# Kernel optimization log

Hardware: AMD Instinct MI355X
Metric: run time of the kernel (lower is better)

## Reference

```python
import jax, jax.numpy as jnp
import numpy as np

RES = 7          # POOLER_RESOLUTION
SR = 2           # POOLER_SAMPLING_RATIO
SCALES = (0.25, 0.125, 0.0625, 0.03125)
CANONICAL_SCALE = 224.0
CANONICAL_LEVEL = 4.0
K_MIN, K_MAX = 2.0, 5.0  # -log2(SCALES[0]), -log2(SCALES[-1])


def setup_inputs() -> dict:
    key = jax.random.key(0)
    ks = jax.random.split(key, 9)
    feat0 = jax.random.normal(ks[0], (2, 256, 200, 200), dtype=jnp.float32)
    feat1 = jax.random.normal(ks[1], (2, 256, 100, 100), dtype=jnp.float32)
    feat2 = jax.random.normal(ks[2], (2, 256, 50, 50), dtype=jnp.float32)
    feat3 = jax.random.normal(ks[3], (2, 256, 25, 25), dtype=jnp.float32)
    R = 512
    x1 = jax.random.uniform(ks[4], (R,)) * 600.0
    y1 = jax.random.uniform(ks[5], (R,)) * 600.0
    w = 16.0 + jax.random.uniform(ks[6], (R,)) * 500.0
    h = 16.0 + jax.random.uniform(ks[7], (R,)) * 500.0
    boxes = jnp.stack([x1, y1, x1 + w, y1 + h], axis=1).astype(jnp.float32)
    batch_idx = jax.random.randint(ks[8], (R,), 0, 2, dtype=jnp.int32)
    return {"feat0": feat0, "feat1": feat1, "feat2": feat2, "feat3": feat3,
            "boxes": boxes, "batch_idx": batch_idx}


def _map_levels(boxes):
    # LevelMapper: floor(k0 + log2(sqrt(area)/224 + eps)), clamp to [k_min,k_max], shift
    area = jnp.maximum(boxes[:, 2] - boxes[:, 0], 0.0) * jnp.maximum(boxes[:, 3] - boxes[:, 1], 0.0)
    s = jnp.sqrt(area)
    lvl = jnp.floor(CANONICAL_LEVEL + jnp.log2(s / CANONICAL_SCALE + 1e-6))
    return (jnp.clip(lvl, K_MIN, K_MAX) - K_MIN).astype(jnp.int32)


def _roi_align(feat, boxes, batch_idx, scale):
    # feat: [B,C,H,W]; boxes: [R,4] (x1,y1,x2,y2) in image coords; ROIAlign (aligned=False)
    H, W = feat.shape[2], feat.shape[3]
    x1 = boxes[:, 0] * scale
    y1 = boxes[:, 1] * scale
    x2 = boxes[:, 2] * scale
    y2 = boxes[:, 3] * scale
    roi_w = jnp.maximum(x2 - x1, 1.0)
    roi_h = jnp.maximum(y2 - y1, 1.0)
    bin_w = roi_w / RES
    bin_h = roi_h / RES
    # sample-point offsets within the roi, in bin units: [RES*SR]
    p = (jnp.arange(RES, dtype=jnp.float32)[:, None]
         + (jnp.arange(SR, dtype=jnp.float32)[None, :] + 0.5) / SR).reshape(-1)
    ys = y1[:, None] + p[None, :] * bin_h[:, None]   # [R,S]
    xs = x1[:, None] + p[None, :] * bin_w[:, None]   # [R,S]
    valid_y = (ys >= -1.0) & (ys <= float(H))
    valid_x = (xs >= -1.0) & (xs <= float(W))
    yc = jnp.clip(ys, 0.0, float(H - 1))
    xc = jnp.clip(xs, 0.0, float(W - 1))
    y0 = jnp.floor(yc).astype(jnp.int32)
    x0 = jnp.floor(xc).astype(jnp.int32)
    y1i = jnp.minimum(y0 + 1, H - 1)
    x1i = jnp.minimum(x0 + 1, W - 1)
    ly = yc - y0.astype(jnp.float32)
    lx = xc - x0.astype(jnp.float32)
    hy = 1.0 - ly
    hx = 1.0 - lx
    b = batch_idx[:, None, None]  # [R,1,1]

    def gather(yi, xi):
        # advanced indexing -> [R,S,S,C]
        return feat[b, :, yi[:, :, None], xi[:, None, :]]

    v = (gather(y0, x0) * (hy[:, :, None] * hx[:, None, :])[..., None]
         + gather(y0, x1i) * (hy[:, :, None] * lx[:, None, :])[..., None]
         + gather(y1i, x0) * (ly[:, :, None] * hx[:, None, :])[..., None]
         + gather(y1i, x1i) * (ly[:, :, None] * lx[:, None, :])[..., None])
    v = v * (valid_y[:, :, None] & valid_x[:, None, :])[..., None].astype(v.dtype)
    R = boxes.shape[0]
    C = feat.shape[1]
    v = v.reshape(R, RES, SR, RES, SR, C).mean(axis=(2, 4))  # [R,RES,RES,C]
    return jnp.transpose(v, (0, 3, 1, 2))  # [R,C,RES,RES]


def reference(feat0, feat1, feat2, feat3, boxes, batch_idx):
    feats = (feat0, feat1, feat2, feat3)
    levels = _map_levels(boxes)
    out = jnp.zeros((boxes.shape[0], feat0.shape[1], RES, RES), dtype=feat0.dtype)
    for lvl, (f, sc) in enumerate(zip(feats, SCALES)):
        pooled = _roi_align(f, boxes, batch_idx, sc)
        out = out + jnp.where((levels == lvl)[:, None, None, None], pooled, 0.0)
    return out
```

## Files before the change

### kernel.cpp

```cpp
#include <hip/hip_runtime.h>
#include <hip/hip_bf16.h>

#define RES 7
#define NCH 256

__device__ __forceinline__ unsigned short f32_to_bf16_rne(float f) {
    unsigned int u = __float_as_uint(f);
    u += 0x7fffu + ((u >> 16) & 1u);
    return (unsigned short)(u >> 16);
}

__device__ __forceinline__ unsigned int pack_bf16x2(float lo, float hi) {
    return (unsigned int)f32_to_bf16_rne(lo) | ((unsigned int)f32_to_bf16_rne(hi) << 16);
}

__global__ __launch_bounds__(512) void transpose_all_bf16_v3(
    const float* __restrict__ f0, const float* __restrict__ f1,
    const float* __restrict__ f2, const float* __restrict__ f3,
    unsigned short* __restrict__ ws)
{
    __shared__ unsigned short lds[64 * 260];

    const int t  = threadIdx.x;
    const int hq = t & 15;
    const int cr = t >> 4;
    const int w  = t >> 6;
    const int ln = t & 63;

    for (int id = blockIdx.x; id < 1664; id += 832) {
        const int b = (id >= 832) ? 1 : 0;
        const int x = id - (b ? 832 : 0);

        const int l    = (x >= 625) + (x >= 782) + (x >= 822);
        const int base = (l == 0) ? 0 : (l == 1) ? 625 : (l == 2) ? 782 : 822;
        const int HW   = (l == 0) ? 40000 : (l == 1) ? 10000 : (l == 2) ? 2500 : 625;
        const float* __restrict__ src =
            (l == 0) ? f0 : (l == 1) ? f1 : (l == 2) ? f2 : f3;
        const size_t doff = (l == 0) ? 0u : (l == 1) ? 20480000u
                          : (l == 2) ? 25600000u : 26880000u;

        const int hw0 = (x - base) * 64;
        const float* __restrict__ s    = src + (size_t)b * NCH * HW;
        unsigned short* __restrict__ d = ws + doff + (size_t)b * HW * NCH;
        const int hwq = hw0 + 4 * hq;

#pragma unroll
        for (int g = 0; g < 2; ++g) {
            const int c0 = 4 * cr + 128 * g;
            float va[4][4];
            if (hwq + 3 < HW) {
#pragma unroll
                for (int i = 0; i < 4; ++i) {
                    const float4 f = *(const float4*)(s + (size_t)(c0 + i) * HW + hwq);
                    va[i][0] = f.x; va[i][1] = f.y; va[i][2] = f.z; va[i][3] = f.w;
                }
            } else {
#pragma unroll
                for (int i = 0; i < 4; ++i)
#pragma unroll
                    for (int j = 0; j < 4; ++j)
                        va[i][j] = (hwq + j < HW) ? s[(size_t)(c0 + i) * HW + hwq + j] : 0.0f;
            }
#pragma unroll
            for (int j = 0; j < 4; ++j) {
                uint2 p;
                p.x = pack_bf16x2(va[0][j], va[1][j]);
                p.y = pack_bf16x2(va[2][j], va[3][j]);
                *(uint2*)&lds[(4 * hq + j) * 260 + c0] = p;
            }
        }
        __syncthreads();

#pragma unroll
        for (int j = 0; j < 8; ++j) {
            const int hwl = w + 8 * j;
            const int hw  = hw0 + hwl;
            if (hw < HW) {
                const uint2 p = *(const uint2*)&lds[hwl * 260 + 4 * ln];
                *(uint2*)(d + (size_t)hw * NCH + 4 * ln) = p;
            }
        }
        __syncthreads();
    }
}

__global__ __launch_bounds__(512) void roi_gather_nhwc_bf16(
    const unsigned short* __restrict__ ws,
    const float* __restrict__ boxes, const int* __restrict__ bidx,
    float* __restrict__ out)
{
    __shared__ float lds[49 * 260];

    const int r   = blockIdx.x;
    const int t   = threadIdx.x;
    const int cq  = t & 63;
    const int grp = t >> 6;

    const float bx1 = boxes[r * 4 + 0];
    const float by1 = boxes[r * 4 + 1];
    const float bx2 = boxes[r * 4 + 2];
    const float by2 = boxes[r * 4 + 3];

    const float area = fmaxf(bx2 - bx1, 0.0f) * fmaxf(by2 - by1, 0.0f);
    const float s    = sqrtf(area);
    const float lvlf = floorf(4.0f + log2f(s / 224.0f + 1e-6f));
    const int   lvl  = (int)(fminf(fmaxf(lvlf, 2.0f), 5.0f)) - 2;

    float scale; int H; size_t off;
    if      (lvl == 0) { scale = 0.25f;    H = 200; off = 0u; }
    else if (lvl == 1) { scale = 0.125f;   H = 100; off = 20480000u; }
    else if (lvl == 2) { scale = 0.0625f;  H = 50;  off = 25600000u; }
    else               { scale = 0.03125f; H = 25;  off = 26880000u; }
    const int W = H;

    const int b = bidx[r];
    const unsigned short* __restrict__ feat = ws + off + (size_t)b * H * W * NCH;

    const float x1 = bx1 * scale;
    const float y1 = by1 * scale;
    const float roi_w = fmaxf(bx2 * scale - x1, 1.0f);
    const float roi_h = fmaxf(by2 * scale - y1, 1.0f);
    const float bw = roi_w * (1.0f / RES);
    const float bh = roi_h * (1.0f / RES);

    for (int bin = grp; bin < 49; bin += 8) {
        const int py = bin / 7;
        const int px = bin - py * 7;

        float acc0 = 0.0f, acc1 = 0.0f, acc2 = 0.0f, acc3 = 0.0f;
#pragma unroll
        for (int sy = 0; sy < 2; ++sy) {
            const float pyf = (float)py + ((float)sy + 0.5f) * 0.5f;
            const float ysmp = y1 + pyf * bh;
            const bool  vy   = (ysmp >= -1.0f) && (ysmp <= (float)H);
            const float ycl  = fminf(fmaxf(ysmp, 0.0f), (float)(H - 1));
            const int   y0   = (int)floorf(ycl);
            const int   y1i  = min(y0 + 1, H - 1);
            const float ly   = ycl - (float)y0;
            const float hy   = 1.0f - ly;
#pragma unroll
            for (int sx = 0; sx < 2; ++sx) {
                const float pxf = (float)px + ((float)sx + 0.5f) * 0.5f;
                const float xsmp = x1 + pxf * bw;
                const bool  vx   = (xsmp >= -1.0f) && (xsmp <= (float)W);
                const float xcl  = fminf(fmaxf(xsmp, 0.0f), (float)(W - 1));
                const int   x0   = (int)floorf(xcl);
                const int   x1i  = min(x0 + 1, W - 1);
                const float lx   = xcl - (float)x0;
                const float hx   = 1.0f - lx;

                const float m   = (vy && vx) ? 1.0f : 0.0f;
                const float w00 = m * hy * hx;
                const float w01 = m * hy * lx;
                const float w10 = m * ly * hx;
                const float w11 = m * ly * lx;

                const uint2 u00 = *(const uint2*)(feat + ((size_t)(y0  * W + x0 )) * NCH + 4 * cq);
                const uint2 u01 = *(const uint2*)(feat + ((size_t)(y0  * W + x1i)) * NCH + 4 * cq);
                const uint2 u10 = *(const uint2*)(feat + ((size_t)(y1i * W + x0 )) * NCH + 4 * cq);
                const uint2 u11 = *(const uint2*)(feat + ((size_t)(y1i * W + x1i)) * NCH + 4 * cq);

                acc0 += w00 * __uint_as_float(u00.x << 16)
                      + w01 * __uint_as_float(u01.x << 16)
                      + w10 * __uint_as_float(u10.x << 16)
                      + w11 * __uint_as_float(u11.x << 16);
                acc1 += w00 * __uint_as_float(u00.x & 0xffff0000u)
                      + w01 * __uint_as_float(u01.x & 0xffff0000u)
                      + w10 * __uint_as_float(u10.x & 0xffff0000u)
                      + w11 * __uint_as_float(u11.x & 0xffff0000u);
                acc2 += w00 * __uint_as_float(u00.y << 16)
                      + w01 * __uint_as_float(u01.y << 16)
                      + w10 * __uint_as_float(u10.y << 16)
                      + w11 * __uint_as_float(u11.y << 16);
                acc3 += w00 * __uint_as_float(u00.y & 0xffff0000u)
                      + w01 * __uint_as_float(u01.y & 0xffff0000u)
                      + w10 * __uint_as_float(u10.y & 0xffff0000u)
                      + w11 * __uint_as_float(u11.y & 0xffff0000u);
            }
        }
        float4* dst = (float4*)&lds[bin * 260 + 4 * cq];
        *dst = make_float4(acc0 * 0.25f, acc1 * 0.25f, acc2 * 0.25f, acc3 * 0.25f);
    }

    __syncthreads();

    float* __restrict__ o = out + (size_t)r * (NCH * 49);
    for (int i = t; i < NCH * 49; i += 512) {
        const int ch = i / 49;
        const int bn = i - ch * 49;
        o[i] = lds[bn * 260 + ch];
    }
}

__global__ __launch_bounds__(256) void roi_align_fpn_kernel(
    const float* __restrict__ f0, const float* __restrict__ f1,
    const float* __restrict__ f2, const float* __restrict__ f3,
    const float* __restrict__ boxes, const int* __restrict__ bidx,
    float* __restrict__ out)
{
    const int r   = blockIdx.x;
    const int bin = blockIdx.y;
    const int c   = threadIdx.x;
    const int py  = bin / RES;
    const int px  = bin - py * RES;

    const float bx1 = boxes[r * 4 + 0];
    const float by1 = boxes[r * 4 + 1];
    const float bx2 = boxes[r * 4 + 2];
    const float by2 = boxes[r * 4 + 3];

    const float area = fmaxf(bx2 - bx1, 0.0f) * fmaxf(by2 - by1, 0.0f);
    const float s    = sqrtf(area);
    const float lvlf = floorf(4.0f + log2f(s / 224.0f + 1e-6f));
    const int   lvl  = (int)(fminf(fmaxf(lvlf, 2.0f), 5.0f)) - 2;

    const float scales[4] = {0.25f, 0.125f, 0.0625f, 0.03125f};
    const int   Hs[4]     = {200, 100, 50, 25};
    const float* feats[4] = {f0, f1, f2, f3};

    const float scale = scales[lvl];
    const int   H     = Hs[lvl];
    const int   W     = H;
    const float* feat = feats[lvl];

    const int b = bidx[r];

    const float x1 = bx1 * scale;
    const float y1 = by1 * scale;
    const float roi_w = fmaxf(bx2 * scale - x1, 1.0f);
    const float roi_h = fmaxf(by2 * scale - y1, 1.0f);
    const float bw = roi_w * (1.0f / RES);
    const float bh = roi_h * (1.0f / RES);

    const float* __restrict__ fc = feat + (size_t)(b * NCH + c) * H * W;

    float acc = 0.0f;
#pragma unroll
    for (int sy = 0; sy < 2; ++sy) {
        const float pyf = (float)py + ((float)sy + 0.5f) * 0.5f;
        const float ys  = y1 + pyf * bh;
        const bool  vy  = (ys >= -1.0f) && (ys <= (float)H);
        const float ycl = fminf(fmaxf(ys, 0.0f), (float)(H - 1));
        const int   y0  = (int)floorf(ycl);
        const int   y1i = min(y0 + 1, H - 1);
        const float ly  = ycl - (float)y0;
        const float hy  = 1.0f - ly;
#pragma unroll
        for (int sx = 0; sx < 2; ++sx) {
            const float pxf = (float)px + ((float)sx + 0.5f) * 0.5f;
            const float xs  = x1 + pxf * bw;
            const bool  vx  = (xs >= -1.0f) && (xs <= (float)W);
            const float xcl = fminf(fmaxf(xs, 0.0f), (float)(W - 1));
            const int   x0  = (int)floorf(xcl);
            const int   x1i = min(x0 + 1, W - 1);
            const float lx  = xcl - (float)x0;
            const float hx  = 1.0f - lx;

            const float v00 = fc[y0  * W + x0 ];
            const float v01 = fc[y0  * W + x1i];
            const float v10 = fc[y1i * W + x0 ];
            const float v11 = fc[y1i * W + x1i];

            const float v = v00 * (hy * hx) + v01 * (hy * lx)
                          + v10 * (ly * hx) + v11 * (ly * lx);
            if (vy && vx) acc += v;
        }
    }

    out[((size_t)r * NCH + c) * (RES * RES) + bin] = acc * 0.25f;
}

extern "C" void kernel_launch(void* const* d_in, const int* in_sizes, int n_in,
                              void* d_out, int out_size, void* d_ws, size_t ws_size,
                              hipStream_t stream)
{
    const float* f0    = (const float*)d_in[0];
    const float* f1    = (const float*)d_in[1];
    const float* f2    = (const float*)d_in[2];
    const float* f3    = (const float*)d_in[3];
    const float* boxes = (const float*)d_in[4];
    const int*   bidx  = (const int*)d_in[5];
    float* out = (float*)d_out;

    const int R = in_sizes[4] / 4;

    const size_t need = 27200000ull * sizeof(unsigned short);

    if (ws_size >= need) {
        unsigned short* ws = (unsigned short*)d_ws;
        transpose_all_bf16_v3<<<dim3(832), dim3(512), 0, stream>>>(f0, f1, f2, f3, ws);
        roi_gather_nhwc_bf16<<<dim3(R), dim3(512), 0, stream>>>(ws, boxes, bidx, out);
    } else {
        dim3 grid(R, RES * RES);
        roi_align_fpn_kernel<<<grid, dim3(NCH), 0, stream>>>(f0, f1, f2, f3, boxes, bidx, out);
    }
}
```

Measured before the change: 51.73 us.

## Transpose only feature tiles touched by ROIs using a planning bitmap

Adds a planning kernel that computes each ROI's sampled footprint per level and batch, then marks the 64-pixel tiles it touches in a bitmap. The transpose-to-NHWC-bf16 kernel now launches one block per tile and exits early for unmarked tiles, so feature regions no ROI samples are not converted. This trades a memset and a small extra kernel, plus serialized atomics in the planner, for less HBM traffic in the transpose. Common ROI parameter math is factored into a shared helper.

```diff
diff --git a/kernel.cpp b/kernel.cpp
--- a/kernel.cpp
+++ b/kernel.cpp
@@ -3,6 +3,10 @@
 
 #define RES 7
 #define NCH 256
+
+#define WS_BF16_ELEMS 27200000ull
+#define BM_OFFSET_BYTES 54400000ull
+#define NTILES 1664
 
 __device__ __forceinline__ unsigned short f32_to_bf16_rne(float f) {
     unsigned int u = __float_as_uint(f);
@@ -14,73 +18,125 @@
     return (unsigned int)f32_to_bf16_rne(lo) | ((unsigned int)f32_to_bf16_rne(hi) << 16);
 }
 
-__global__ __launch_bounds__(512) void transpose_all_bf16_v3(
+__device__ __forceinline__ void roi_params(
+    const float* __restrict__ boxes, int r,
+    int& k, float& scale, int& H, float& x1, float& y1, float& bw, float& bh)
+{
+    const float bx1 = boxes[r * 4 + 0];
+    const float by1 = boxes[r * 4 + 1];
+    const float bx2 = boxes[r * 4 + 2];
+    const float by2 = boxes[r * 4 + 3];
+    const float area = fmaxf(bx2 - bx1, 0.0f) * fmaxf(by2 - by1, 0.0f);
+    const float s    = sqrtf(area);
+    const float lvlf = floorf(4.0f + log2f(s / 224.0f + 1e-6f));
+    k = (int)(fminf(fmaxf(lvlf, 2.0f), 5.0f)) - 2;
+    if      (k == 0) { scale = 0.25f;    H = 200; }
+    else if (k == 1) { scale = 0.125f;   H = 100; }
+    else if (k == 2) { scale = 0.0625f;  H = 50;  }
+    else             { scale = 0.03125f; H = 25;  }
+    x1 = bx1 * scale;
+    y1 = by1 * scale;
+    const float roi_w = fmaxf(bx2 * scale - x1, 1.0f);
+    const float roi_h = fmaxf(by2 * scale - y1, 1.0f);
+    bw = roi_w * (1.0f / RES);
+    bh = roi_h * (1.0f / RES);
+}
+
+__global__ __launch_bounds__(512) void roi_plan(
+    const float* __restrict__ boxes, const int* __restrict__ bidx, int R,
+    unsigned int* __restrict__ bitmap)
+{
+    for (int r = blockIdx.x * 512 + threadIdx.x; r < R; r += gridDim.x * 512) {
+        int k, H; float scale, x1, y1, bw, bh;
+        roi_params(boxes, r, k, scale, H, x1, y1, bw, bh);
+        const int W = H;
+        const int base = (k == 0) ? 0 : (k == 1) ? 625 : (k == 2) ? 782 : 822;
+        const int tb   = bidx[r] * 832 + base;
+
+        const float ys_lo = fminf(fmaxf(y1 + 0.25f * bh, 0.0f), (float)(H - 1));
+        const float ys_hi = fminf(fmaxf(y1 + 6.75f * bh, 0.0f), (float)(H - 1));
+        const float xs_lo = fminf(fmaxf(x1 + 0.25f * bw, 0.0f), (float)(W - 1));
+        const float xs_hi = fminf(fmaxf(x1 + 6.75f * bw, 0.0f), (float)(W - 1));
+        const int yA = max((int)floorf(ys_lo) - 1, 0);
+        const int yB = min((int)floorf(ys_hi) + 2, H - 1);
+        const int xA = max((int)floorf(xs_lo) - 1, 0);
+        const int xB = min((int)floorf(xs_hi) + 2, W - 1);
+
+        for (int y = yA; y <= yB; ++y) {
+            const int t0 = (y * W + xA) >> 6;
+            const int t1 = (y * W + xB) >> 6;
+            for (int t = t0; t <= t1; ++t) atomicOr(&bitmap[tb + t], 1u);
+        }
+    }
+}
+
+__global__ __launch_bounds__(512) void transpose_sel_bf16(
     const float* __restrict__ f0, const float* __restrict__ f1,
     const float* __restrict__ f2, const float* __restrict__ f3,
-    unsigned short* __restrict__ ws)
-{
+    unsigned short* __restrict__ ws, const unsigned int* __restrict__ bitmap)
+{
+    const int id = blockIdx.x;
+    if (bitmap && bitmap[id] == 0u) return;
+
     __shared__ unsigned short lds[64 * 260];
 
-    const int t  = threadIdx.x;
-    const int hq = t & 15;
-    const int cr = t >> 4;
+    const int b = (id >= 832) ? 1 : 0;
+    const int x = id - (b ? 832 : 0);
+
+    const int l    = (x >= 625) + (x >= 782) + (x >= 822);
+    const int base = (l == 0) ? 0 : (l == 1) ? 625 : (l == 2) ? 782 : 822;
+    const int HW   = (l == 0) ? 40000 : (l == 1) ? 10000 : (l == 2) ? 2500 : 625;
+    const float* __restrict__ src =
+        (l == 0) ? f0 : (l == 1) ? f1 : (l == 2) ? f2 : f3;
+    const size_t doff = (l == 0) ? 0u : (l == 1) ? 20480000u
+                      : (l == 2) ? 25600000u : 26880000u;
+
+    const int hw0 = (x - base) * 64;
+    const float* __restrict__ s    = src + (size_t)b * NCH * HW;
+    unsigned short* __restrict__ d = ws + doff + (size_t)b * HW * NCH;
+
+    const int t   = threadIdx.x;
+    const int hq  = t & 15;
+    const int cr  = t >> 4;
+    const int hwq = hw0 + 4 * hq;
+
+#pragma unroll
+    for (int g = 0; g < 2; ++g) {
+        const int c0 = 4 * cr + 128 * g;
+        float va[4][4];
+        if (hwq + 3 < HW) {
+#pragma unroll
+            for (int i = 0; i < 4; ++i) {
+                const float4 f = *(const float4*)(s + (size_t)(c0 + i) * HW + hwq);
+                va[i][0] = f.x; va[i][1] = f.y; va[i][2] = f.z; va[i][3] = f.w;
+            }
+        } else {
+#pragma unroll
+            for (int i = 0; i < 4; ++i)
+#pragma unroll
+                for (int j = 0; j < 4; ++j)
+                    va[i][j] = (hwq + j < HW) ? s[(size_t)(c0 + i) * HW + hwq + j] : 0.0f;
+        }
+#pragma unroll
+        for (int j = 0; j < 4; ++j) {
+            uint2 p;
+            p.x = pack_bf16x2(va[0][j], va[1][j]);
+            p.y = pack_bf16x2(va[2][j], va[3][j]);
+            *(uint2*)&lds[(4 * hq + j) * 260 + c0] = p;
+        }
+    }
+    __syncthreads();
+
     const int w  = t >> 6;
     const int ln = t & 63;
-
-    for (int id = blockIdx.x; id < 1664; id += 832) {
-        const int b = (id >= 832) ? 1 : 0;
-        const int x = id - (b ? 832 : 0);
-
-        const int l    = (x >= 625) + (x >= 782) + (x >= 822);
-        const int base = (l == 0) ? 0 : (l == 1) ? 625 : (l == 2) ? 782 : 822;
-        const int HW   = (l == 0) ? 40000 : (l == 1) ? 10000 : (l == 2) ? 2500 : 625;
-        const float* __restrict__ src =
-            (l == 0) ? f0 : (l == 1) ? f1 : (l == 2) ? f2 : f3;
-        const size_t doff = (l == 0) ? 0u : (l == 1) ? 20480000u
-                          : (l == 2) ? 25600000u : 26880000u;
-
-        const int hw0 = (x - base) * 64;
-        const float* __restrict__ s    = src + (size_t)b * NCH * HW;
-        unsigned short* __restrict__ d = ws + doff + (size_t)b * HW * NCH;
-        const int hwq = hw0 + 4 * hq;
-
-#pragma unroll
-        for (int g = 0; g < 2; ++g) {
-            const int c0 = 4 * cr + 128 * g;
-            float va[4][4];
-            if (hwq + 3 < HW) {
-#pragma unroll
-                for (int i = 0; i < 4; ++i) {
-                    const float4 f = *(const float4*)(s + (size_t)(c0 + i) * HW + hwq);
-                    va[i][0] = f.x; va[i][1] = f.y; va[i][2] = f.z; va[i][3] = f.w;
-                }
-            } else {
-#pragma unroll
-                for (int i = 0; i < 4; ++i)
-#pragma unroll
-                    for (int j = 0; j < 4; ++j)
-                        va[i][j] = (hwq + j < HW) ? s[(size_t)(c0 + i) * HW + hwq + j] : 0.0f;
-            }
-#pragma unroll
-            for (int j = 0; j < 4; ++j) {
-                uint2 p;
-                p.x = pack_bf16x2(va[0][j], va[1][j]);
-                p.y = pack_bf16x2(va[2][j], va[3][j]);
-                *(uint2*)&lds[(4 * hq + j) * 260 + c0] = p;
-            }
-        }
-        __syncthreads();
-
-#pragma unroll
-        for (int j = 0; j < 8; ++j) {
-            const int hwl = w + 8 * j;
-            const int hw  = hw0 + hwl;
-            if (hw < HW) {
-                const uint2 p = *(const uint2*)&lds[hwl * 260 + 4 * ln];
-                *(uint2*)(d + (size_t)hw * NCH + 4 * ln) = p;
-            }
-        }
-        __syncthreads();
+#pragma unroll
+    for (int j = 0; j < 8; ++j) {
+        const int hwl = w + 8 * j;
+        const int hw  = hw0 + hwl;
+        if (hw < HW) {
+            const uint2 p = *(const uint2*)&lds[hwl * 260 + 4 * ln];
+            *(uint2*)(d + (size_t)hw * NCH + 4 * ln) = p;
+        }
     }
 }
 
@@ -96,32 +152,14 @@
     const int cq  = t & 63;
     const int grp = t >> 6;
 
-    const float bx1 = boxes[r * 4 + 0];
-    const float by1 = boxes[r * 4 + 1];
-    const float bx2 = boxes[r * 4 + 2];
-    const float by2 = boxes[r * 4 + 3];
-
-    const float area = fmaxf(bx2 - bx1, 0.0f) * fmaxf(by2 - by1, 0.0f);
-    const float s    = sqrtf(area);
-    const float lvlf = floorf(4.0f + log2f(s / 224.0f + 1e-6f));
-    const int   lvl  = (int)(fminf(fmaxf(lvlf, 2.0f), 5.0f)) - 2;
-
-    float scale; int H; size_t off;
-    if      (lvl == 0) { scale = 0.25f;    H = 200; off = 0u; }
-    else if (lvl == 1) { scale = 0.125f;   H = 100; off = 20480000u; }
-    else if (lvl == 2) { scale = 0.0625f;  H = 50;  off = 25600000u; }
-    else               { scale = 0.03125f; H = 25;  off = 26880000u; }
+    int k, H; float scale, x1, y1, bw, bh;
+    roi_params(boxes, r, k, scale, H, x1, y1, bw, bh);
     const int W = H;
+    const size_t off = (k == 0) ? 0u : (k == 1) ? 20480000u
+                     : (k == 2) ? 25600000u : 26880000u;
 
     const int b = bidx[r];
     const unsigned short* __restrict__ feat = ws + off + (size_t)b * H * W * NCH;
-
-    const float x1 = bx1 * scale;
-    const float y1 = by1 * scale;
-    const float roi_w = fmaxf(bx2 * scale - x1, 1.0f);
-    const float roi_h = fmaxf(by2 * scale - y1, 1.0f);
-    const float bw = roi_w * (1.0f / RES);
-    const float bh = roi_h * (1.0f / RES);
 
     for (int bin = grp; bin < 49; bin += 8) {
         const int py = bin / 7;
@@ -204,33 +242,12 @@
     const int py  = bin / RES;
     const int px  = bin - py * RES;
 
-    const float bx1 = boxes[r * 4 + 0];
-    const float by1 = boxes[r * 4 + 1];
-    const float bx2 = boxes[r * 4 + 2];
-    const float by2 = boxes[r * 4 + 3];
-
-    const float area = fmaxf(bx2 - bx1, 0.0f) * fmaxf(by2 - by1, 0.0f);
-    const float s    = sqrtf(area);
-    const float lvlf = floorf(4.0f + log2f(s / 224.0f + 1e-6f));
-    const int   lvl  = (int)(fminf(fmaxf(lvlf, 2.0f), 5.0f)) - 2;
-
-    const float scales[4] = {0.25f, 0.125f, 0.0625f, 0.03125f};
-    const int   Hs[4]     = {200, 100, 50, 25};
+    int k, H; float scale, x1, y1, bw, bh;
+    roi_params(boxes, r, k, scale, H, x1, y1, bw, bh);
+    const int W = H;
     const float* feats[4] = {f0, f1, f2, f3};
-
-    const float scale = scales[lvl];
-    const int   H     = Hs[lvl];
-    const int   W     = H;
-    const float* feat = feats[lvl];
-
+    const float* feat = feats[k];
     const int b = bidx[r];
-
-    const float x1 = bx1 * scale;
-    const float y1 = by1 * scale;
-    const float roi_w = fmaxf(bx2 * scale - x1, 1.0f);
-    const float roi_h = fmaxf(by2 * scale - y1, 1.0f);
-    const float bw = roi_w * (1.0f / RES);
-    const float bh = roi_h * (1.0f / RES);
 
     const float* __restrict__ fc = feat + (size_t)(b * NCH + c) * H * W;
 
@@ -284,11 +301,19 @@
 
     const int R = in_sizes[4] / 4;
 
-    const size_t need = 27200000ull * sizeof(unsigned short);
-
-    if (ws_size >= need) {
+    const size_t need_ws = WS_BF16_ELEMS * sizeof(unsigned short);
+    const size_t need_bm = BM_OFFSET_BYTES + NTILES * sizeof(unsigned int);
+
+    if (ws_size >= need_ws) {
         unsigned short* ws = (unsigned short*)d_ws;
-        transpose_all_bf16_v3<<<dim3(832), dim3(512), 0, stream>>>(f0, f1, f2, f3, ws);
+        unsigned int* bitmap = nullptr;
+        if (ws_size >= need_bm) {
+            bitmap = (unsigned int*)((char*)d_ws + BM_OFFSET_BYTES);
+            hipMemsetAsync(bitmap, 0, NTILES * sizeof(unsigned int), stream);
+            roi_plan<<<dim3(2), dim3(512), 0, stream>>>(boxes, bidx, R, bitmap);
+        }
+        transpose_sel_bf16<<<dim3(NTILES), dim3(512), 0, stream>>>(
+            f0, f1, f2, f3, ws, bitmap);
         roi_gather_nhwc_bf16<<<dim3(R), dim3(512), 0, stream>>>(ws, boxes, bidx, out);
     } else {
         dim3 grid(R, RES * RES);
```

Result: slower. 81.25 us (+57.1%).
